# Optimization experiments

Hardware: AMD Instinct MI355X
Metric: run time of the kernel (lower is better)

Reference implementation:

```python
import jax, jax.numpy as jnp
import numpy as np

NUM_HEADS = 12
HEAD_DIM = 64
HIDDEN = 768
BATCH = 2
SEQ = 2048
NEG_BIG = 1e12


def _rope_tables(seq_len, dim, dtype=jnp.float32):
    # theta_i = 10000^(-2i/dim); sin/cos repeat-interleaved -> [seq_len, dim]
    half = dim // 2
    theta = jnp.power(10000.0, -jnp.arange(half, dtype=dtype) * (2.0 / dim))
    ang = jnp.arange(seq_len, dtype=dtype)[:, None] * theta[None, :]  # [n, half]
    sin_pos = jnp.repeat(jnp.sin(ang), 2, axis=-1)  # [n, dim]
    cos_pos = jnp.repeat(jnp.cos(ang), 2, axis=-1)
    return sin_pos, cos_pos


def setup_inputs() -> dict:
    key = jax.random.key(0)
    k1, k2, k3, k4 = jax.random.split(key, 4)
    inputs = jax.random.normal(k1, (BATCH, SEQ, HIDDEN), dtype=jnp.float32)
    mask = jax.random.randint(k2, (BATCH, SEQ), 0, 2, dtype=jnp.int32)
    # nn.Linear(hidden, num_heads*head_dim*2): weight [out, in], bias [out]
    W = jax.random.normal(k3, (NUM_HEADS * HEAD_DIM * 2, HIDDEN), dtype=jnp.float32) * (HIDDEN ** -0.5)
    b = jax.random.normal(k4, (NUM_HEADS * HEAD_DIM * 2,), dtype=jnp.float32) * 0.02
    return {"inputs": inputs, "mask": mask, "W": W, "b": b}


def reference(inputs, mask, W, b):
    B, N, _ = inputs.shape
    H, D = NUM_HEADS, HEAD_DIM
    hs = jnp.einsum('bnh,oh->bno', inputs, W) + b          # [B, N, 2*H*D]
    hs = hs.reshape(B, N, H, 2 * D)                        # split+stack -> [B, N, H, 2D]
    qw, kw = hs[..., :D], hs[..., D:]                      # [B, N, H, D]
    # qw2 = cat([-q_odd, q_even], -1) as in the torch code
    qw2 = jnp.concatenate([-qw[..., 1::2], qw[..., ::2]], axis=-1)
    kw2 = jnp.concatenate([-kw[..., 1::2], kw[..., ::2]], axis=-1)
    # permute to [B, H, N, D]
    qw, qw2 = qw.transpose(0, 2, 1, 3), qw2.transpose(0, 2, 1, 3)
    kw, kw2 = kw.transpose(0, 2, 1, 3), kw2.transpose(0, 2, 1, 3)
    sin_pos, cos_pos = _rope_tables(N, D, hs.dtype)        # [N, D], broadcasts over B, H
    qw = qw * cos_pos + qw2 * sin_pos
    kw = kw * cos_pos + kw2 * sin_pos
    logits = jnp.einsum('bhnd,bhmd->bhnm', qw, kw)         # [B, H, N, N]
    # padding mask over key axis: mask [B,N] -> [B,1,1,N]
    pad = mask.astype(logits.dtype)[:, None, None, :]
    logits = logits * pad - (1.0 - pad) * NEG_BIG
    # strictly-lower-triangular mask (keep upper triangle + diagonal)
    tril = jnp.tril(jnp.ones((N, N), dtype=logits.dtype), k=-1)
    logits = logits - tril * NEG_BIG
    return logits / (D ** 0.5)
```

## Files before the change

### kernel.cpp

```cpp
#include <hip/hip_runtime.h>
#include <hip/hip_bf16.h>
#include <cmath>

#define NH   12
#define HD   64
#define HID  768
#define NB   2
#define SEQL 2048
#define ROWS 4096
#define OUTW 1536

static constexpr float NEGBIG = 1000000000000.0f;

typedef __attribute__((ext_vector_type(4)))  float f32x4;
typedef __attribute__((ext_vector_type(8)))  short short8;
typedef __attribute__((ext_vector_type(16))) float f32x16;

__device__ __forceinline__ unsigned short f2bf(float f) {
    unsigned int u = __builtin_bit_cast(unsigned int, f);
    u += 0x7FFFu + ((u >> 16) & 1u);
    return (unsigned short)(u >> 16);
}

#define XQ (ROWS * HID / 4)
#define WQ (OUTW * HID / 4)
#define RQ (SEQL * 32)
__global__ void k_prep(const float* __restrict__ X, const float* __restrict__ W,
                       unsigned short* __restrict__ Xbf, unsigned short* __restrict__ Wbf,
                       float2* __restrict__ rtab) {
    int i = blockIdx.x * blockDim.x + threadIdx.x;
    if (i < XQ + WQ) {
        const float* src = (i < XQ) ? X : W;
        unsigned short* dst = (i < XQ) ? Xbf : Wbf;
        int k = (i < XQ) ? i : i - XQ;
        float4 v = reinterpret_cast<const float4*>(src)[k];
        ushort4 o;
        o.x = f2bf(v.x); o.y = f2bf(v.y); o.z = f2bf(v.z); o.w = f2bf(v.w);
        reinterpret_cast<ushort4*>(dst)[k] = o;
    } else if (i < XQ + WQ + RQ) {
        int idx = i - (XQ + WQ);
        int n = idx >> 5, d = idx & 31;
        float theta = exp2f(-(float)d * (13.287712379549449f / 32.0f));
        float ang = (float)n * theta;
        rtab[idx] = make_float2(sinf(ang), cosf(ang));
    }
}

__global__ __launch_bounds__(256, 3) void k_proj_rope(
    const unsigned short* __restrict__ Xbf,
    const unsigned short* __restrict__ Wbf,
    const float*  __restrict__ bias,
    const float2* __restrict__ rtab,
    unsigned short* __restrict__ Qbf,
    unsigned short* __restrict__ Kbf)
{
    const int bid = blockIdx.x;
    const int newbid = (bid & 7) * 96 + (bid >> 3);
    const int slab = newbid / 12;
    const int head = newbid % 12;
    const int row0 = slab * 64;
    const int tid  = threadIdx.x;
    const int lane = tid & 63;
    const int w    = tid >> 6;
    const int wr = w & 1, wc = w >> 1;
    const int l31 = lane & 31, lhi = lane >> 5;
    const int x7  = l31 & 7;

    __shared__ __align__(16) unsigned short smem[24576];

    f32x16 acc[2];
    {
        float bj0 = bias[head * 128 + wc * 64 + l31];
        float bj1 = bias[head * 128 + wc * 64 + 32 + l31];
#pragma unroll
        for (int r = 0; r < 16; ++r) { acc[0][r] = bj0; acc[1][r] = bj1; }
    }

    const unsigned short* Abase = Xbf + (size_t)row0 * HID;
    const unsigned short* Bbase = Wbf + (size_t)(head * 128) * HID;

    short8 ga[2], gb[4];
#pragma unroll
    for (int r = 0; r < 2; ++r) {
        int idx = tid + 256 * r, row = idx >> 3, s = idx & 7;
        ga[r] = *reinterpret_cast<const short8*>(Abase + (size_t)row * HID + s * 8);
    }
#pragma unroll
    for (int r = 0; r < 4; ++r) {
        int idx = tid + 256 * r, row = idx >> 3, s = idx & 7;
        gb[r] = *reinterpret_cast<const short8*>(Bbase + (size_t)row * HID + s * 8);
    }
#pragma unroll
    for (int r = 0; r < 2; ++r) {
        int idx = tid + 256 * r, row = idx >> 3, s = idx & 7, ws = s ^ (row & 7);
        *reinterpret_cast<short8*>(smem + row * 64 + ws * 8) = ga[r];
    }
#pragma unroll
    for (int r = 0; r < 4; ++r) {
        int idx = tid + 256 * r, row = idx >> 3, s = idx & 7, ws = s ^ (row & 7);
        *reinterpret_cast<short8*>(smem + 8192 + row * 64 + ws * 8) = gb[r];
    }
    __syncthreads();

    for (int t = 0; t < 12; ++t) {
        const int cur = t & 1;
        if (t < 11) {
            const int kk = (t + 1) * 64;
#pragma unroll
            for (int r = 0; r < 2; ++r) {
                int idx = tid + 256 * r, row = idx >> 3, s = idx & 7;
                ga[r] = *reinterpret_cast<const short8*>(Abase + (size_t)row * HID + kk + s * 8);
            }
#pragma unroll
            for (int r = 0; r < 4; ++r) {
                int idx = tid + 256 * r, row = idx >> 3, s = idx & 7;
                gb[r] = *reinterpret_cast<const short8*>(Bbase + (size_t)row * HID + kk + s * 8);
            }
        }
        const unsigned short* Ab = smem + cur * 4096;
        const unsigned short* Bb = smem + 8192 + cur * 8192;
#pragma unroll
        for (int ks = 0; ks < 4; ++ks) {
            int sl = (ks * 2 + lhi) ^ x7;
            short8 a  = *reinterpret_cast<const short8*>(Ab + (wr * 32 + l31) * 64      + sl * 8);
            short8 b0 = *reinterpret_cast<const short8*>(Bb + (wc * 64 + l31) * 64      + sl * 8);
            short8 b1 = *reinterpret_cast<const short8*>(Bb + (wc * 64 + 32 + l31) * 64 + sl * 8);
            acc[0] = __builtin_amdgcn_mfma_f32_32x32x16_bf16(a, b0, acc[0], 0, 0, 0);
            acc[1] = __builtin_amdgcn_mfma_f32_32x32x16_bf16(a, b1, acc[1], 0, 0, 0);
        }
        if (t < 11) {
            const int nxt = cur ^ 1;
#pragma unroll
            for (int r = 0; r < 2; ++r) {
                int idx = tid + 256 * r, row = idx >> 3, s = idx & 7, ws = s ^ (row & 7);
                *reinterpret_cast<short8*>(smem + nxt * 4096 + row * 64 + ws * 8) = ga[r];
            }
#pragma unroll
            for (int r = 0; r < 4; ++r) {
                int idx = tid + 256 * r, row = idx >> 3, s = idx & 7, ws = s ^ (row & 7);
                *reinterpret_cast<short8*>(smem + 8192 + nxt * 8192 + row * 64 + ws * 8) = gb[r];
            }
        }
        __syncthreads();
    }

    float (*hs)[132] = reinterpret_cast<float (*)[132]>(smem);
#pragma unroll
    for (int j = 0; j < 2; ++j)
#pragma unroll
        for (int r = 0; r < 16; ++r) {
            int rr = (r & 3) + 8 * (r >> 2) + 4 * lhi;
            hs[wr * 32 + rr][wc * 64 + j * 32 + l31] = acc[j][r];
        }
    __syncthreads();
#pragma unroll 4
    for (int it = 0; it < 16; ++it) {
        int f   = tid + 256 * it;
        int row = f >> 6;
        int u   = f & 63;
        int isK = u >> 5;
        int dp  = u & 31;
        int d0  = 2 * dp, d1 = d0 + 1;
        int cb  = isK * 64;
        int grow = row0 + row;
        int bI = grow >> 11;
        int n  = grow & 2047;
        float2 sc = rtab[n * 32 + dp];
        float v0 = hs[row][cb + d0];
        float v1 = hs[row][cb + d1];
        int p0 = (d0 < 32) ? (2 * d0 + 1) : (2 * d0 - 64);
        int p1 = (d1 < 32) ? (2 * d1 + 1) : (2 * d1 - 64);
        float pv0 = hs[row][cb + p0];
        float pv1 = hs[row][cb + p1];
        float sg0 = (d0 < 32) ? -1.0f : 1.0f;
        float sg1 = (d1 < 32) ? -1.0f : 1.0f;
        ushort2 st;
        st.x = f2bf(v0 * sc.y + sg0 * pv0 * sc.x);
        st.y = f2bf(v1 * sc.y + sg1 * pv1 * sc.x);
        unsigned short* dst = isK ? (unsigned short*)Kbf : (unsigned short*)Qbf;
        size_t idx = ((size_t)(bI * NH + head) * SEQL + n) * HD + d0;
        *reinterpret_cast<ushort2*>(dst + idx) = st;
    }
}

__global__ __launch_bounds__(256) void k_logits(
    const unsigned short* __restrict__ Qbf,
    const unsigned short* __restrict__ Kbf,
    const int* __restrict__ mask,
    float* __restrict__ out)
{
    const int bid = blockIdx.x;
    const int newbid = (bid & 7) * 768 + (bid >> 3);
    const int bh = newbid >> 8;
    const int t  = newbid & 255;
    const int nt = t >> 4, mt = t & 15;
    const int bI = bh / NH;
    const int tid = threadIdx.x;
    float* outbase = out + (size_t)bh * SEQL * SEQL;

    if (mt < nt) {
        const int cg = tid & 31;
        const int r0 = tid >> 5;
        const int m0 = mt * 128 + cg * 4;
        const int4 mi = *reinterpret_cast<const int4*>(mask + bI * SEQL + m0);
        f32x4 v;
        v.x = ((float)mi.x - 2.0f) * (NEGBIG * 0.125f);
        v.y = ((float)mi.y - 2.0f) * (NEGBIG * 0.125f);
        v.z = ((float)mi.z - 2.0f) * (NEGBIG * 0.125f);
        v.w = ((float)mi.w - 2.0f) * (NEGBIG * 0.125f);
        float* ob = outbase + (size_t)(nt * 128) * SEQL + m0;
#pragma unroll
        for (int j = 0; j < 16; ++j) {
            int row = r0 + 8 * j;
            __builtin_nontemporal_store(v, reinterpret_cast<f32x4*>(ob + (size_t)row * SEQL));
        }
        return;
    }

    const int lane = tid & 63;
    const int w = tid >> 6;
    const int rowHalf = w & 1, colHalf = w >> 1;
    const int l31 = lane & 31, lhi = lane >> 5;
    const int n0 = nt * 128 + rowHalf * 64;
    const int m0 = mt * 128 + colHalf * 64;

    f32x16 acc[2][2];
#pragma unroll
    for (int i = 0; i < 2; ++i)
#pragma unroll
        for (int j = 0; j < 2; ++j)
#pragma unroll
            for (int r = 0; r < 16; ++r) acc[i][j][r] = 0.0f;

    const unsigned short* Aq = Qbf + ((size_t)bh * SEQL + n0 + l31) * HD + 8 * lhi;
    const unsigned short* Bk = Kbf + ((size_t)bh * SEQL + m0 + l31) * HD + 8 * lhi;
#pragma unroll
    for (int t2 = 0; t2 < 4; ++t2) {
        short8 a0 = *reinterpret_cast<const short8*>(Aq + 16 * t2);
        short8 a1 = *reinterpret_cast<const short8*>(Aq + 32 * HD + 16 * t2);
        short8 b0 = *reinterpret_cast<const short8*>(Bk + 16 * t2);
        short8 b1 = *reinterpret_cast<const short8*>(Bk + 32 * HD + 16 * t2);
        acc[0][0] = __builtin_amdgcn_mfma_f32_32x32x16_bf16(a0, b0, acc[0][0], 0, 0, 0);
        acc[0][1] = __builtin_amdgcn_mfma_f32_32x32x16_bf16(a0, b1, acc[0][1], 0, 0, 0);
        acc[1][0] = __builtin_amdgcn_mfma_f32_32x32x16_bf16(a1, b0, acc[1][0], 0, 0, 0);
        acc[1][1] = __builtin_amdgcn_mfma_f32_32x32x16_bf16(a1, b1, acc[1][1], 0, 0, 0);
    }

    __shared__ float tl[64][128];
#pragma unroll
    for (int i = 0; i < 2; ++i) {
#pragma unroll
        for (int j = 0; j < 2; ++j) {
#pragma unroll
            for (int r = 0; r < 16; ++r) {
                int rr = (r & 3) + 8 * (r >> 2) + 4 * lhi;
                tl[rowHalf * 32 + rr][colHalf * 64 + j * 32 + l31] = acc[i][j][r];
            }
        }
        __syncthreads();
#pragma unroll
        for (int it = 0; it < 8; ++it) {
            int f   = tid + 256 * it;
            int lr  = f >> 5;
            int cg  = f & 31;
            int grow = nt * 128 + (lr >> 5) * 64 + i * 32 + (lr & 31);
            int gcol = mt * 128 + cg * 4;
            const int4 mi = *reinterpret_cast<const int4*>(mask + bI * SEQL + gcol);
            f32x4 v = *reinterpret_cast<const f32x4*>(&tl[lr][cg * 4]);
            float pads[4] = {(float)mi.x, (float)mi.y, (float)mi.z, (float)mi.w};
#pragma unroll
            for (int e = 0; e < 4; ++e) {
                float vv = v[e] * pads[e] - (1.0f - pads[e]) * NEGBIG;
                if (gcol + e < grow) vv -= NEGBIG;
                v[e] = vv * 0.125f;
            }
            __builtin_nontemporal_store(v, reinterpret_cast<f32x4*>(outbase + (size_t)grow * SEQL + gcol));
        }
        __syncthreads();
    }
}

extern "C" void kernel_launch(void* const* d_in, const int* in_sizes, int n_in,
                              void* d_out, int out_size, void* d_ws, size_t ws_size,
                              hipStream_t stream) {
    const float* x    = (const float*)d_in[0];
    const int*   mask = (const int*)d_in[1];
    const float* W    = (const float*)d_in[2];
    const float* bias = (const float*)d_in[3];
    float* out = (float*)d_out;

    char* ws = (char*)d_ws;
    unsigned short* Xbf = (unsigned short*)(ws);
    unsigned short* Wbf = (unsigned short*)(ws + 6291456);
    unsigned short* Qbf = (unsigned short*)(ws + 8650752);
    unsigned short* Kbf = (unsigned short*)(ws + 14942208);
    float2*         rtab = (float2*)(ws + 21233664);

    const int prep_items = XQ + WQ + RQ;
    k_prep<<<dim3((prep_items + 255) / 256), dim3(256), 0, stream>>>(x, W, Xbf, Wbf, rtab);
    k_proj_rope<<<dim3(768), dim3(256), 0, stream>>>(Xbf, Wbf, bias, rtab, Qbf, Kbf);
    k_logits<<<dim3(6144), dim3(256), 0, stream>>>(Qbf, Kbf, mask, out);
}
```

Before: 104.6 us.

## Move strictly-lower tile fills into projection kernel and shrink logits grid

The constant-fill work for the strictly-lower-triangular 128x128 tiles (which depends only on the mask) moves out of the logits kernel and into the projection kernel as 2880 extra blocks, so those large output writes can overlap with the projection GEMM. The logits kernel then launches only the 136 upper-triangle tiles per batch-head and decodes triangular tile indices with a small loop. The projection path also drops to single-buffered shared memory with extra barriers and a two-pass epilogue, halving LDS use to allow higher occupancy (launch bounds 4). The trade-off is serialized load/compute within each projection block and index-decoding loops in both kernels.

Result: faster. 93.22 us (-10.9%).

```diff
diff --git a/kernel.cpp b/kernel.cpp
--- a/kernel.cpp
+++ b/kernel.cpp
@@ -46,159 +46,28 @@
     }
 }
 
-__global__ __launch_bounds__(256, 3) void k_proj_rope(
+__global__ __launch_bounds__(256, 4) void k_proj_fill(
     const unsigned short* __restrict__ Xbf,
     const unsigned short* __restrict__ Wbf,
     const float*  __restrict__ bias,
     const float2* __restrict__ rtab,
     unsigned short* __restrict__ Qbf,
-    unsigned short* __restrict__ Kbf)
-{
-    const int bid = blockIdx.x;
-    const int newbid = (bid & 7) * 96 + (bid >> 3);
-    const int slab = newbid / 12;
-    const int head = newbid % 12;
-    const int row0 = slab * 64;
-    const int tid  = threadIdx.x;
-    const int lane = tid & 63;
-    const int w    = tid >> 6;
-    const int wr = w & 1, wc = w >> 1;
-    const int l31 = lane & 31, lhi = lane >> 5;
-    const int x7  = l31 & 7;
-
-    __shared__ __align__(16) unsigned short smem[24576];
-
-    f32x16 acc[2];
-    {
-        float bj0 = bias[head * 128 + wc * 64 + l31];
-        float bj1 = bias[head * 128 + wc * 64 + 32 + l31];
-#pragma unroll
-        for (int r = 0; r < 16; ++r) { acc[0][r] = bj0; acc[1][r] = bj1; }
-    }
-
-    const unsigned short* Abase = Xbf + (size_t)row0 * HID;
-    const unsigned short* Bbase = Wbf + (size_t)(head * 128) * HID;
-
-    short8 ga[2], gb[4];
-#pragma unroll
-    for (int r = 0; r < 2; ++r) {
-        int idx = tid + 256 * r, row = idx >> 3, s = idx & 7;
-        ga[r] = *reinterpret_cast<const short8*>(Abase + (size_t)row * HID + s * 8);
-    }
-#pragma unroll
-    for (int r = 0; r < 4; ++r) {
-        int idx = tid + 256 * r, row = idx >> 3, s = idx & 7;
-        gb[r] = *reinterpret_cast<const short8*>(Bbase + (size_t)row * HID + s * 8);
-    }
-#pragma unroll
-    for (int r = 0; r < 2; ++r) {
-        int idx = tid + 256 * r, row = idx >> 3, s = idx & 7, ws = s ^ (row & 7);
-        *reinterpret_cast<short8*>(smem + row * 64 + ws * 8) = ga[r];
-    }
-#pragma unroll
-    for (int r = 0; r < 4; ++r) {
-        int idx = tid + 256 * r, row = idx >> 3, s = idx & 7, ws = s ^ (row & 7);
-        *reinterpret_cast<short8*>(smem + 8192 + row * 64 + ws * 8) = gb[r];
-    }
-    __syncthreads();
-
-    for (int t = 0; t < 12; ++t) {
-        const int cur = t & 1;
-        if (t < 11) {
-            const int kk = (t + 1) * 64;
-#pragma unroll
-            for (int r = 0; r < 2; ++r) {
-                int idx = tid + 256 * r, row = idx >> 3, s = idx & 7;
-                ga[r] = *reinterpret_cast<const short8*>(Abase + (size_t)row * HID + kk + s * 8);
-            }
-#pragma unroll
-            for (int r = 0; r < 4; ++r) {
-                int idx = tid + 256 * r, row = idx >> 3, s = idx & 7;
-                gb[r] = *reinterpret_cast<const short8*>(Bbase + (size_t)row * HID + kk + s * 8);
-            }
-        }
-        const unsigned short* Ab = smem + cur * 4096;
-        const unsigned short* Bb = smem + 8192 + cur * 8192;
-#pragma unroll
-        for (int ks = 0; ks < 4; ++ks) {
-            int sl = (ks * 2 + lhi) ^ x7;
-            short8 a  = *reinterpret_cast<const short8*>(Ab + (wr * 32 + l31) * 64      + sl * 8);
-            short8 b0 = *reinterpret_cast<const short8*>(Bb + (wc * 64 + l31) * 64      + sl * 8);
-            short8 b1 = *reinterpret_cast<const short8*>(Bb + (wc * 64 + 32 + l31) * 64 + sl * 8);
-            acc[0] = __builtin_amdgcn_mfma_f32_32x32x16_bf16(a, b0, acc[0], 0, 0, 0);
-            acc[1] = __builtin_amdgcn_mfma_f32_32x32x16_bf16(a, b1, acc[1], 0, 0, 0);
-        }
-        if (t < 11) {
-            const int nxt = cur ^ 1;
-#pragma unroll
-            for (int r = 0; r < 2; ++r) {
-                int idx = tid + 256 * r, row = idx >> 3, s = idx & 7, ws = s ^ (row & 7);
-                *reinterpret_cast<short8*>(smem + nxt * 4096 + row * 64 + ws * 8) = ga[r];
-            }
-#pragma unroll
-            for (int r = 0; r < 4; ++r) {
-                int idx = tid + 256 * r, row = idx >> 3, s = idx & 7, ws = s ^ (row & 7);
-                *reinterpret_cast<short8*>(smem + 8192 + nxt * 8192 + row * 64 + ws * 8) = gb[r];
-            }
-        }
-        __syncthreads();
-    }
-
-    float (*hs)[132] = reinterpret_cast<float (*)[132]>(smem);
-#pragma unroll
-    for (int j = 0; j < 2; ++j)
-#pragma unroll
-        for (int r = 0; r < 16; ++r) {
-            int rr = (r & 3) + 8 * (r >> 2) + 4 * lhi;
-            hs[wr * 32 + rr][wc * 64 + j * 32 + l31] = acc[j][r];
-        }
-    __syncthreads();
-#pragma unroll 4
-    for (int it = 0; it < 16; ++it) {
-        int f   = tid + 256 * it;
-        int row = f >> 6;
-        int u   = f & 63;
-        int isK = u >> 5;
-        int dp  = u & 31;
-        int d0  = 2 * dp, d1 = d0 + 1;
-        int cb  = isK * 64;
-        int grow = row0 + row;
-        int bI = grow >> 11;
-        int n  = grow & 2047;
-        float2 sc = rtab[n * 32 + dp];
-        float v0 = hs[row][cb + d0];
-        float v1 = hs[row][cb + d1];
-        int p0 = (d0 < 32) ? (2 * d0 + 1) : (2 * d0 - 64);
-        int p1 = (d1 < 32) ? (2 * d1 + 1) : (2 * d1 - 64);
-        float pv0 = hs[row][cb + p0];
-        float pv1 = hs[row][cb + p1];
-        float sg0 = (d0 < 32) ? -1.0f : 1.0f;
-        float sg1 = (d1 < 32) ? -1.0f : 1.0f;
-        ushort2 st;
-        st.x = f2bf(v0 * sc.y + sg0 * pv0 * sc.x);
-        st.y = f2bf(v1 * sc.y + sg1 * pv1 * sc.x);
-        unsigned short* dst = isK ? (unsigned short*)Kbf : (unsigned short*)Qbf;
-        size_t idx = ((size_t)(bI * NH + head) * SEQL + n) * HD + d0;
-        *reinterpret_cast<ushort2*>(dst + idx) = st;
-    }
-}
-
-__global__ __launch_bounds__(256) void k_logits(
-    const unsigned short* __restrict__ Qbf,
-    const unsigned short* __restrict__ Kbf,
+    unsigned short* __restrict__ Kbf,
     const int* __restrict__ mask,
     float* __restrict__ out)
 {
     const int bid = blockIdx.x;
-    const int newbid = (bid & 7) * 768 + (bid >> 3);
-    const int bh = newbid >> 8;
-    const int t  = newbid & 255;
-    const int nt = t >> 4, mt = t & 15;
-    const int bI = bh / NH;
     const int tid = threadIdx.x;
-    float* outbase = out + (size_t)bh * SEQL * SEQL;
-
-    if (mt < nt) {
+
+    if (bid >= 768) {
+        const int fid = bid - 768;
+        const int bh  = fid / 120;
+        int j = fid % 120;
+        int ntv = 1;
+        while (j >= ntv) { j -= ntv; ++ntv; }
+        const int nt = ntv, mt = j;
+        const int bI = bh / NH;
+        float* outbase = out + (size_t)bh * SEQL * SEQL;
         const int cg = tid & 31;
         const int r0 = tid >> 5;
         const int m0 = mt * 128 + cg * 4;
@@ -210,12 +79,158 @@
         v.w = ((float)mi.w - 2.0f) * (NEGBIG * 0.125f);
         float* ob = outbase + (size_t)(nt * 128) * SEQL + m0;
 #pragma unroll
-        for (int j = 0; j < 16; ++j) {
-            int row = r0 + 8 * j;
+        for (int jj = 0; jj < 16; ++jj) {
+            int row = r0 + 8 * jj;
             __builtin_nontemporal_store(v, reinterpret_cast<f32x4*>(ob + (size_t)row * SEQL));
         }
         return;
     }
+
+    const int newbid = (bid & 7) * 96 + (bid >> 3);
+    const int slab = newbid / 12;
+    const int head = newbid % 12;
+    const int row0 = slab * 64;
+    const int lane = tid & 63;
+    const int w    = tid >> 6;
+    const int wr = w & 1, wc = w >> 1;
+    const int l31 = lane & 31, lhi = lane >> 5;
+    const int x7  = l31 & 7;
+
+    __shared__ __align__(16) unsigned short smem[12288];
+
+    f32x16 acc[2];
+    {
+        float bj0 = bias[head * 128 + wc * 64 + l31];
+        float bj1 = bias[head * 128 + wc * 64 + 32 + l31];
+#pragma unroll
+        for (int r = 0; r < 16; ++r) { acc[0][r] = bj0; acc[1][r] = bj1; }
+    }
+
+    const unsigned short* Abase = Xbf + (size_t)row0 * HID;
+    const unsigned short* Bbase = Wbf + (size_t)(head * 128) * HID;
+
+    short8 ga[2], gb[4];
+#pragma unroll
+    for (int r = 0; r < 2; ++r) {
+        int idx = tid + 256 * r, row = idx >> 3, s = idx & 7;
+        ga[r] = *reinterpret_cast<const short8*>(Abase + (size_t)row * HID + s * 8);
+    }
+#pragma unroll
+    for (int r = 0; r < 4; ++r) {
+        int idx = tid + 256 * r, row = idx >> 3, s = idx & 7;
+        gb[r] = *reinterpret_cast<const short8*>(Bbase + (size_t)row * HID + s * 8);
+    }
+#pragma unroll
+    for (int r = 0; r < 2; ++r) {
+        int idx = tid + 256 * r, row = idx >> 3, s = idx & 7, ws = s ^ (row & 7);
+        *reinterpret_cast<short8*>(smem + row * 64 + ws * 8) = ga[r];
+    }
+#pragma unroll
+    for (int r = 0; r < 4; ++r) {
+        int idx = tid + 256 * r, row = idx >> 3, s = idx & 7, ws = s ^ (row & 7);
+        *reinterpret_cast<short8*>(smem + 4096 + row * 64 + ws * 8) = gb[r];
+    }
+
+    for (int t = 0; t < 12; ++t) {
+        __syncthreads();
+        if (t < 11) {
+            const int kk = (t + 1) * 64;
+#pragma unroll
+            for (int r = 0; r < 2; ++r) {
+                int idx = tid + 256 * r, row = idx >> 3, s = idx & 7;
+                ga[r] = *reinterpret_cast<const short8*>(Abase + (size_t)row * HID + kk + s * 8);
+            }
+#pragma unroll
+            for (int r = 0; r < 4; ++r) {
+                int idx = tid + 256 * r, row = idx >> 3, s = idx & 7;
+                gb[r] = *reinterpret_cast<const short8*>(Bbase + (size_t)row * HID + kk + s * 8);
+            }
+        }
+#pragma unroll
+        for (int ks = 0; ks < 4; ++ks) {
+            int sl = (ks * 2 + lhi) ^ x7;
+            short8 a  = *reinterpret_cast<const short8*>(smem + (wr * 32 + l31) * 64 + sl * 8);
+            short8 b0 = *reinterpret_cast<const short8*>(smem + 4096 + (wc * 64 + l31) * 64 + sl * 8);
+            short8 b1 = *reinterpret_cast<const short8*>(smem + 4096 + (wc * 64 + 32 + l31) * 64 + sl * 8);
+            acc[0] = __builtin_amdgcn_mfma_f32_32x32x16_bf16(a, b0, acc[0], 0, 0, 0);
+            acc[1] = __builtin_amdgcn_mfma_f32_32x32x16_bf16(a, b1, acc[1], 0, 0, 0);
+        }
+        if (t < 11) {
+            __syncthreads();
+#pragma unroll
+            for (int r = 0; r < 2; ++r) {
+                int idx = tid + 256 * r, row = idx >> 3, s = idx & 7, ws = s ^ (row & 7);
+                *reinterpret_cast<short8*>(smem + row * 64 + ws * 8) = ga[r];
+            }
+#pragma unroll
+            for (int r = 0; r < 4; ++r) {
+                int idx = tid + 256 * r, row = idx >> 3, s = idx & 7, ws = s ^ (row & 7);
+                *reinterpret_cast<short8*>(smem + 4096 + row * 64 + ws * 8) = gb[r];
+            }
+        }
+    }
+    __syncthreads();
+
+    float (*hs)[132] = reinterpret_cast<float (*)[132]>(smem);
+    for (int s = 0; s < 2; ++s) {
+        if (wr == s) {
+#pragma unroll
+            for (int j = 0; j < 2; ++j)
+#pragma unroll
+                for (int r = 0; r < 16; ++r) {
+                    int rr = (r & 3) + 8 * (r >> 2) + 4 * lhi;
+                    hs[rr][wc * 64 + j * 32 + l31] = acc[j][r];
+                }
+        }
+        __syncthreads();
+#pragma unroll 4
+        for (int it = 0; it < 8; ++it) {
+            int f   = tid + 256 * it;
+            int row = f >> 6;
+            int u   = f & 63;
+            int isK = u >> 5;
+            int dp  = u & 31;
+            int d0  = 2 * dp, d1 = d0 + 1;
+            int cb  = isK * 64;
+            int grow = row0 + s * 32 + row;
+            int bI = grow >> 11;
+            int n  = grow & 2047;
+            float2 sc = rtab[n * 32 + dp];
+            float v0 = hs[row][cb + d0];
+            float v1 = hs[row][cb + d1];
+            int p0 = (d0 < 32) ? (2 * d0 + 1) : (2 * d0 - 64);
+            int p1 = (d1 < 32) ? (2 * d1 + 1) : (2 * d1 - 64);
+            float pv0 = hs[row][cb + p0];
+            float pv1 = hs[row][cb + p1];
+            float sg0 = (d0 < 32) ? -1.0f : 1.0f;
+            float sg1 = (d1 < 32) ? -1.0f : 1.0f;
+            ushort2 st;
+            st.x = f2bf(v0 * sc.y + sg0 * pv0 * sc.x);
+            st.y = f2bf(v1 * sc.y + sg1 * pv1 * sc.x);
+            unsigned short* dst = isK ? (unsigned short*)Kbf : (unsigned short*)Qbf;
+            size_t idx = ((size_t)(bI * NH + head) * SEQL + n) * HD + d0;
+            *reinterpret_cast<ushort2*>(dst + idx) = st;
+        }
+        __syncthreads();
+    }
+}
+
+__global__ __launch_bounds__(256) void k_logits(
+    const unsigned short* __restrict__ Qbf,
+    const unsigned short* __restrict__ Kbf,
+    const int* __restrict__ mask,
+    float* __restrict__ out)
+{
+    const int bid = blockIdx.x;
+    const int newbid = (bid & 7) * 408 + (bid >> 3);
+    const int bh = newbid / 136;
+    int j = newbid % 136;
+    int ntv = 0;
+    while (j >= 16 - ntv) { j -= 16 - ntv; ++ntv; }
+    const int nt = ntv, mt = ntv + j;
+    const int bI = bh / NH;
+    const int tid = threadIdx.x;
+    float* outbase = out + (size_t)bh * SEQL * SEQL;
 
     const int lane = tid & 63;
     const int w = tid >> 6;
@@ -228,9 +243,9 @@
 #pragma unroll
     for (int i = 0; i < 2; ++i)
 #pragma unroll
-        for (int j = 0; j < 2; ++j)
-#pragma unroll
-            for (int r = 0; r < 16; ++r) acc[i][j][r] = 0.0f;
+        for (int jj = 0; jj < 2; ++jj)
+#pragma unroll
+            for (int r = 0; r < 16; ++r) acc[i][jj][r] = 0.0f;
 
     const unsigned short* Aq = Qbf + ((size_t)bh * SEQL + n0 + l31) * HD + 8 * lhi;
     const unsigned short* Bk = Kbf + ((size_t)bh * SEQL + m0 + l31) * HD + 8 * lhi;
@@ -250,11 +265,11 @@
 #pragma unroll
     for (int i = 0; i < 2; ++i) {
 #pragma unroll
-        for (int j = 0; j < 2; ++j) {
+        for (int jj = 0; jj < 2; ++jj) {
 #pragma unroll
             for (int r = 0; r < 16; ++r) {
                 int rr = (r & 3) + 8 * (r >> 2) + 4 * lhi;
-                tl[rowHalf * 32 + rr][colHalf * 64 + j * 32 + l31] = acc[i][j][r];
+                tl[rowHalf * 32 + rr][colHalf * 64 + jj * 32 + l31] = acc[i][jj][r];
             }
         }
         __syncthreads();
@@ -298,6 +313,6 @@
 
     const int prep_items = XQ + WQ + RQ;
     k_prep<<<dim3((prep_items + 255) / 256), dim3(256), 0, stream>>>(x, W, Xbf, Wbf, rtab);
-    k_proj_rope<<<dim3(768), dim3(256), 0, stream>>>(Xbf, Wbf, bias, rtab, Qbf, Kbf);
-    k_logits<<<dim3(6144), dim3(256), 0, stream>>>(Qbf, Kbf, mask, out);
-}
+    k_proj_fill<<<dim3(3648), dim3(256), 0, stream>>>(Xbf, Wbf, bias, rtab, Qbf, Kbf, mask, out);
+    k_logits<<<dim3(3264), dim3(256), 0, stream>>>(Qbf, Kbf, mask, out);
+}
```
